# Kernel tuning notes

Hardware: AMD Instinct MI355X
Metric: run time of the kernel (lower is better)

## Reference

```python
import jax, jax.numpy as jnp
import numpy as np

D_MODEL = 1024
EXPAND = 2
D_INNER = D_MODEL * EXPAND  # 2048
C = 8
B, T = 4, 2048


def setup_inputs() -> dict:
    key = jax.random.key(0)
    ks = jax.random.split(key, 8)
    x = jax.random.normal(ks[0], (B, T, D_MODEL), jnp.float32)
    # omega init: uniform in [a, b] per the torch code
    a = np.log(1.0 / np.exp(np.log(0.999) / C) - 1.0)
    b = np.log(1.0 / np.exp(np.log(0.9) / C) - 1.0)
    omega = (a + (b - a) * jax.random.uniform(ks[1], (1, 1, D_INNER))).astype(jnp.float32)
    s = 0.02
    Win = (jax.random.normal(ks[2], (2 * D_INNER, D_MODEL)) * s).astype(jnp.float32)   # in_proj, no bias
    Wl = (jax.random.normal(ks[3], (D_INNER, D_INNER)) * s).astype(jnp.float32)        # lambda_proj weight
    bl = jnp.zeros((D_INNER,), jnp.float32)                                            # lambda_proj bias
    Wv = (jax.random.normal(ks[4], (D_INNER, D_INNER)) * s).astype(jnp.float32)        # mixer householder-vector proj
    bv = jnp.zeros((D_INNER,), jnp.float32)
    Wout = (jax.random.normal(ks[5], (D_MODEL, D_INNER)) * s).astype(jnp.float32)      # out_proj, no bias
    return dict(x=x, omega=omega, Win=Win, Wl=Wl, bl=bl, Wv=Wv, bv=bv, Wout=Wout)


def reference(x, omega, Win, Wl, bl, Wv, bv, Wout):
    # in_proj then split into (x, z)
    xz = jnp.einsum('btd,ed->bte', x, Win)              # [B,T,2*D_INNER]
    xi, z = jnp.split(xz, 2, axis=-1)                   # each [B,T,D_INNER]
    # lambda gate (computed for all timesteps at once)
    log_lam = -C * jax.nn.softplus(omega) * jax.nn.sigmoid(jnp.einsum('bti,ji->btj', xi, Wl) + bl)
    lam = jnp.exp(log_lam)                              # [B,T,D_INNER]
    # Householder (rank-1, identity activation) mixer vectors, hoisted out of the scan
    v = jnp.einsum('bti,ji->btj', xi, Wv) + bv          # [B,T,D_INNER]

    h0 = xi[:, 0]                                       # [B,D_INNER]

    def step(h_prev, inp):
        x_t, v_t, lam_t = inp
        vh = jnp.sum(v_t * h_prev, axis=-1, keepdims=True)
        vv = jnp.sum(v_t * v_t, axis=-1, keepdims=True)
        Qh = h_prev - 2.0 * v_t * (vh / vv)             # Householder reflection of h
        h = lam_t * Qh + (1.0 - lam_t) * x_t
        return h, h

    xs = (jnp.swapaxes(xi[:, 1:], 0, 1),                # [T-1,B,D_INNER]
          jnp.swapaxes(v[:, 1:], 0, 1),
          jnp.swapaxes(lam[:, 1:], 0, 1))
    _, hs = jax.lax.scan(step, h0, xs)                  # [T-1,B,D_INNER]
    h = jnp.concatenate([h0[:, None], jnp.swapaxes(hs, 0, 1)], axis=1)  # [B,T,D_INNER]

    return jnp.einsum('bti,di->btd', jax.nn.silu(z) * h, Wout)
```

## Files before the change

### kernel.cpp

```cpp
#include <hip/hip_runtime.h>
#include <cstdint>
#include <cstddef>

typedef unsigned short u16;
typedef __attribute__((ext_vector_type(8))) short s8v;
typedef __attribute__((ext_vector_type(4))) float f4v;
typedef __attribute__((ext_vector_type(2))) float f32x2;

#define D_MODEL 1024
#define D_INNER 2048
#define BT      8192
#define TLEN    2048
#define NBATCH  4

struct alignas(8) U16x4 { u16 x, y, z, w; };

__device__ __forceinline__ u16 f2bf(float f) {
  union { float f; unsigned u; } c; c.f = f;
  unsigned r = c.u + 0x7FFFu + ((c.u >> 16) & 1u);
  return (u16)(r >> 16);
}
__device__ __forceinline__ float blo(unsigned u) {
  union { unsigned u; float f; } c; c.u = u << 16; return c.f;
}
__device__ __forceinline__ float bhi(unsigned u) {
  union { unsigned u; float f; } c; c.u = u & 0xffff0000u; return c.f;
}
__device__ __forceinline__ unsigned pkbf(float lo, float hi) {
  union { float f; unsigned u; } a, b; a.f = lo; b.f = hi;
#if __has_builtin(__builtin_amdgcn_perm)
  return __builtin_amdgcn_perm(b.u + 0x8000u, a.u + 0x8000u, 0x07060302u);
#else
  return ((b.u + 0x8000u) & 0xffff0000u) | ((a.u + 0x8000u) >> 16);
#endif
}

#define DPPADD(x, ctrl) \
  ((x) + __builtin_bit_cast(float, __builtin_amdgcn_update_dpp( \
       0, __builtin_bit_cast(int, (x)), (ctrl), 0xF, 0xF, true)))
__device__ __forceinline__ float wave_sum_dpp(float x) {
  x = DPPADD(x, 0x111);
  x = DPPADD(x, 0x112);
  x = DPPADD(x, 0x114);
  x = DPPADD(x, 0x118);
  x = DPPADD(x, 0x142);
  x = DPPADD(x, 0x143);
  return x;
}

__device__ __forceinline__ void glds16(const u16* g, const u16* lds) {
  __builtin_amdgcn_global_load_lds(
      (const __attribute__((address_space(1))) unsigned int*)(uintptr_t)g,
      (__attribute__((address_space(3))) unsigned int*)(unsigned int)(uintptr_t)lds,
      16, 0, 0);
}

template<int EPI>
__global__ __launch_bounds__(256, 2)
void gemm_nt(const u16* __restrict__ A, const u16* __restrict__ B,
             int M, int N, int K,
             float* __restrict__ Cf, u16* __restrict__ Cb, u16* __restrict__ Cb2,
             const float* __restrict__ bias, const float* __restrict__ sfac,
             const float* __restrict__ bias2)
{
  __shared__ u16 lA[128 * 32];
  __shared__ u16 lB[128 * 32];
  const int tid  = threadIdx.x;
  const int wave = tid >> 6, lane = tid & 63;
  const int wm = wave >> 1, wn = wave & 1;
  const int bm0 = blockIdx.y * 128, bn0 = blockIdx.x * 128;

  const int srow = lane >> 2;
  const int scol = (lane & 3) * 8;
  const u16* pa0 = A + (size_t)(bm0 + wave * 32 + srow) * K + scol;
  const u16* pa1 = pa0 + (size_t)16 * K;
  const u16* pb0 = B + (size_t)(bn0 + wave * 32 + srow) * K + scol;
  const u16* pb1 = pb0 + (size_t)16 * K;
  u16* la0 = lA + (wave * 32) * 32;
  u16* la1 = la0 + 16 * 32;
  u16* lb0 = lB + (wave * 32) * 32;
  u16* lb1 = lb0 + 16 * 32;

  const int fr = lane & 15, kq = lane >> 4;
  const u16* fA = lA + (wm * 64 + fr) * 32 + kq * 8;
  const u16* fB = lB + (wn * 64 + fr) * 32 + kq * 8;

  f4v acc[4][4];
  const f4v zf = {0.f, 0.f, 0.f, 0.f};
  for (int i = 0; i < 4; ++i)
    for (int j = 0; j < 4; ++j)
      acc[i][j] = zf;

  for (int k0 = 0; k0 < K; k0 += 32) {
    glds16(pa0 + k0, la0);
    glds16(pa1 + k0, la1);
    glds16(pb0 + k0, lb0);
    glds16(pb1 + k0, lb1);
    __syncthreads();
    s8v af[4], bfv[4];
#pragma unroll
    for (int i = 0; i < 4; ++i) af[i] = *(const s8v*)(fA + i * 16 * 32);
#pragma unroll
    for (int j = 0; j < 4; ++j) bfv[j] = *(const s8v*)(fB + j * 16 * 32);
// ... 8 lines not shown
#pragma unroll
  for (int i = 0; i < 4; ++i) {
#pragma unroll
    for (int j = 0; j < 4; ++j) {
#pragma unroll
      for (int r = 0; r < 4; ++r) {
        const int gm = bm0 + wm * 64 + i * 16 + kq * 4 + r;
        const int gn = bn0 + wn * 64 + j * 16 + fr;
        const float val = acc[i][j][r];
        if (EPI == 0) {
          if (gn < D_INNER) {
            Cb[(size_t)gm * D_INNER + gn] = f2bf(val);
          } else {
            const float s = val / (1.f + __expf(-val));
            Cb2[(size_t)gm * D_INNER + (gn - D_INNER)] = f2bf(s);
          }
        } else if (EPI == 4) {
          if (gn < D_INNER) {
            const float pre = val + bias[gn];
            const float sig = 1.f / (1.f + __expf(-pre));
            const float m = -expm1f(sfac[gn] * sig);
            Cb2[(size_t)gm * D_INNER + gn] = f2bf(m);
          } else {
            Cb[(size_t)gm * D_INNER + (gn - D_INNER)] = f2bf(val + bias2[gn - D_INNER]);
          }
        } else {
          Cf[(size_t)gm * N + gn] = val;
        }
      }
    }
  }
}

__global__ void conv_bf16_kernel(const float* __restrict__ in, u16* __restrict__ out, int n4)
{
  const int i = blockIdx.x * blockDim.x + threadIdx.x;
  if (i >= n4) return;
  const float4 x = ((const float4*)in)[i];
  U16x4 o; o.x = f2bf(x.x); o.y = f2bf(x.y); o.z = f2bf(x.z); o.w = f2bf(x.w);
  ((U16x4*)out)[i] = o;
}

__global__ void sfac_kernel(const float* __restrict__ omega, float* __restrict__ sfac)
{
  const int i = blockIdx.x * blockDim.x + threadIdx.x;
  if (i < D_INNER) sfac[i] = -8.f * log1pf(expf(omega[i]));
}

__global__ __launch_bounds__(256)
void vscale_kernel(u16* __restrict__ v)
{
  const int row  = blockIdx.x * 4 + (threadIdx.x >> 6);
  const int lane = threadIdx.x & 63;
  uint4* p = (uint4*)(v + (size_t)row * D_INNER + lane * 32);
  uint4 a[4];
#pragma unroll
  for (int i = 0; i < 4; ++i) a[i] = p[i];
  float s = 0.f;
#pragma unroll
  for (int i = 0; i < 4; ++i) {
    const unsigned w[4] = {a[i].x, a[i].y, a[i].z, a[i].w};
#pragma unroll
    for (int j = 0; j < 4; ++j) {
      const float f0 = blo(w[j]), f1 = bhi(w[j]);
      s += f0 * f0 + f1 * f1;
    }
  }
  s += __shfl_down(s, 32); s += __shfl_down(s, 16); s += __shfl_down(s, 8);
  s += __shfl_down(s, 4);  s += __shfl_down(s, 2);  s += __shfl_down(s, 1);
  const float sc = sqrtf(2.f / __shfl(s, 0));
#pragma unroll
  for (int i = 0; i < 4; ++i) {
    const unsigned w[4] = {a[i].x, a[i].y, a[i].z, a[i].w};
    unsigned o[4];
#pragma unroll
    for (int j = 0; j < 4; ++j) o[j] = pkbf(blo(w[j]) * sc, bhi(w[j]) * sc);
    uint4 ov; ov.x = o[0]; ov.y = o[1]; ov.z = o[2]; ov.w = o[3];
    p[i] = ov;
  }
}

__global__ __launch_bounds__(256)
void pairprep_kernel(const u16* __restrict__ vs, const u16* __restrict__ mb,
                     const u16* __restrict__ xi, f32x2* __restrict__ C12)
{
  const int r = blockIdx.x * 4 + (threadIdx.x >> 6);
  const int lane = threadIdx.x & 63;
  const int b = r >> 10;
  const int t = (r & 1023) * 2;
  const size_t o0 = ((size_t)b * TLEN + t) * D_INNER + (size_t)lane * 32;
  const size_t o1 = o0 + D_INNER;
  const uint4* pv0 = (const uint4*)(vs + o0);
  const uint4* pv1 = (const uint4*)(vs + o1);
  const uint4* px0 = (const uint4*)(xi + o0);
  const uint4* pm0 = (const uint4*)(mb + o0);
  float c1 = 0.f, c2 = 0.f;
#pragma unroll
  for (int i = 0; i < 4; ++i) {
    const uint4 v0 = pv0[i], v1 = pv1[i], x0 = px0[i], m0 = pm0[i];
    const unsigned v0w[4] = {v0.x, v0.y, v0.z, v0.w};
    const unsigned v1w[4] = {v1.x, v1.y, v1.z, v1.w};
    const unsigned x0w[4] = {x0.x, x0.y, x0.z, x0.w};
    const unsigned m0w[4] = {m0.x, m0.y, m0.z, m0.w};
#pragma unroll
    for (int q = 0; q < 4; ++q) {
      const float va = blo(v0w[q]), vb = bhi(v0w[q]);
      const float ua = blo(v1w[q]), ub = bhi(v1w[q]);
      const float xa = blo(x0w[q]), xb = bhi(x0w[q]);
      const float ma = blo(m0w[q]), mbv = bhi(m0w[q]);
      const float wa = __builtin_fmaf(-ua, ma, ua);
      const float wb = __builtin_fmaf(-ub, mbv, ub);
      c1 += wa * va + wb * vb;
      c2 += ua * (ma * xa) + ub * (mbv * xb);
    }
  }
  c1 = wave_sum_dpp(c1);
  c2 = wave_sum_dpp(c2);
  if (lane == 63) { f32x2 cc; cc.x = c1; cc.y = c2; C12[r] = cc; }
}

__global__ void zmul_kernel(u16* __restrict__ gh, const u16* __restrict__ sz, int n8)
{
  const int i = blockIdx.x * blockDim.x + threadIdx.x;
  if (i >= n8) return;
  const uint4 hv = ((const uint4*)gh)[i];
  const uint4 zv = ((const uint4*)sz)[i];
  const unsigned hw[4] = {hv.x, hv.y, hv.z, hv.w};
  const unsigned zw[4] = {zv.x, zv.y, zv.z, zv.w};
  unsigned ow[4];
#pragma unroll
  for (int q = 0; q < 4; ++q)
    ow[q] = pkbf(blo(zw[q]) * blo(hw[q]), bhi(zw[q]) * bhi(hw[q]));
  uint4 o; o.x = ow[0]; o.y = ow[1]; o.z = ow[2]; o.w = ow[3];
  ((uint4*)gh)[i] = o;
}

struct Pair {
  uint4 v0, v1, x0, x1, m0, m1;
  f32x2 c;
};

__global__ __launch_bounds__(256, 1)
void scan2_kernel(const u16* __restrict__ xi, const u16* __restrict__ vs,
                  const u16* __restrict__ mb, const f32x2* __restrict__ C12,
                  u16* __restrict__ hb)
{
  const int b = blockIdx.x, tid = threadIdx.x;
  const int wave = tid >> 6, lane = tid & 63;
  const size_t base = (size_t)b * TLEN * D_INNER + (size_t)tid * 8;
  const int cb0 = b * 1024;
  __shared__ __attribute__((aligned(16))) float rP[2][4], rQ[2][4];

  auto load_pair = [&](int t) {
    Pair p;
    const size_t o0 = base + (size_t)t * D_INNER;
    const size_t o1 = o0 + D_INNER;
    p.v0 = *(const uint4*)(vs + o0);
    p.v1 = *(const uint4*)(vs + o1);
    p.x0 = *(const uint4*)(xi + o0);
    p.x1 = *(const uint4*)(xi + o1);
    p.m0 = *(const uint4*)(mb + o0);
    p.m1 = *(const uint4*)(mb + o1);
    p.c = C12[cb0 + (t >> 1)];
    return p;
  };

  float h[8];
  {
    const uint4 x0 = *(const uint4*)(xi + base);
    const unsigned xw[4] = {x0.x, x0.y, x0.z, x0.w};
#pragma unroll
    for (int p = 0; p < 4; ++p) {
      h[2*p]   = blo(xw[p]);
      h[2*p+1] = bhi(xw[p]);
    }
    *(uint4*)(hb + base) = x0;
  }

  {
    const size_t o = base + D_INNER;
    const uint4 v1v = *(const uint4*)(vs + o);
    const uint4 x1v = *(const uint4*)(xi + o);
    const uint4 m1v = *(const uint4*)(mb + o);
    const unsigned vw[4] = {v1v.x, v1v.y, v1v.z, v1v.w};
    float vf[8];
    float P0 = 0.f, P1 = 0.f;
#pragma unroll
    for (int p = 0; p < 4; ++p) {
      vf[2*p]   = blo(vw[p]);
      vf[2*p+1] = bhi(vw[p]);
      P0 = __builtin_fmaf(vf[2*p],   h[2*p],   P0);
      P1 = __builtin_fmaf(vf[2*p+1], h[2*p+1], P1);
    }
    float P = wave_sum_dpp(P0 + P1);
    if (lane == 63) rP[0][wave] = P;
    asm volatile("s_waitcnt lgkmcnt(0)\n\ts_barrier" ::: "memory");
    const float4 sp = *(const float4*)rP[0];
    const float a = (sp.x + sp.y) + (sp.z + sp.w);
    const unsigned xw[4] = {x1v.x, x1v.y, x1v.z, x1v.w};
    const unsigned mw[4] = {m1v.x, m1v.y, m1v.z, m1v.w};
    unsigned ow[4];
#pragma unroll
    for (int p = 0; p < 4; ++p) {
      const float X0 = blo(xw[p]), X1 = bhi(xw[p]);
      const float M0 = blo(mw[p]), M1 = bhi(mw[p]);
      const float t0 = __builtin_fmaf(vf[2*p],   -a, h[2*p]);
      const float t1 = __builtin_fmaf(vf[2*p+1], -a, h[2*p+1]);
      h[2*p]   = __builtin_fmaf(M0, X0 - t0, t0);
      h[2*p+1] = __builtin_fmaf(M1, X1 - t1, t1);
      ow[p] = pkbf(h[2*p], h[2*p+1]);
    }
    uint4 out; out.x = ow[0]; out.y = ow[1]; out.z = ow[2]; out.w = ow[3];
    *(uint4*)(hb + o) = out;
  }

  auto round = [&](const Pair& p, int t) {
    const int par = (t >> 1) & 1;
    const unsigned v0w[4] = {p.v0.x, p.v0.y, p.v0.z, p.v0.w};
    const unsigned v1w[4] = {p.v1.x, p.v1.y, p.v1.z, p.v1.w};
    const unsigned m0w[4] = {p.m0.x, p.m0.y, p.m0.z, p.m0.w};
    float vf[8], uf[8], mf0[8];
    float P0 = 0.f, P1 = 0.f, Q0 = 0.f, Q1 = 0.f;
#pragma unroll
    for (int q = 0; q < 4; ++q) {
      vf[2*q]   = blo(v0w[q]);
      vf[2*q+1] = bhi(v0w[q]);
      uf[2*q]   = blo(v1w[q]);
      uf[2*q+1] = bhi(v1w[q]);
      mf0[2*q]  = blo(m0w[q]);
      mf0[2*q+1]= bhi(m0w[q]);
      const float wa = __builtin_fmaf(-uf[2*q],   mf0[2*q],   uf[2*q]);
      const float wb = __builtin_fmaf(-uf[2*q+1], mf0[2*q+1], uf[2*q+1]);
      P0 = __builtin_fmaf(vf[2*q],   h[2*q],   P0);
      P1 = __builtin_fmaf(vf[2*q+1], h[2*q+1], P1);
      Q0 = __builtin_fmaf(wa, h[2*q],   Q0);
      Q1 = __builtin_fmaf(wb, h[2*q+1], Q1);
    }
    float P = wave_sum_dpp(P0 + P1);
    float Q = wave_sum_dpp(Q0 + Q1);
    if (lane == 63) { rP[par][wave] = P; rQ[par][wave] = Q; }
    asm volatile("s_waitcnt lgkmcnt(0)\n\ts_barrier" ::: "memory");
    const float4 sp = *(const float4*)rP[par];
    const float4 sq = *(const float4*)rQ[par];
    const float a0 = (sp.x + sp.y) + (sp.z + sp.w);
    const float a1 = __builtin_fmaf(-a0, p.c.x, (sq.x + sq.y) + (sq.z + sq.w) + p.c.y);
    const unsigned xw0[4] = {p.x0.x, p.x0.y, p.x0.z, p.x0.w};
    const unsigned xw1[4] = {p.x1.x, p.x1.y, p.x1.z, p.x1.w};
    const unsigned m1w[4] = {p.m1.x, p.m1.y, p.m1.z, p.m1.w};
    unsigned ow0[4], ow1[4];
#pragma unroll
    for (int q = 0; q < 4; ++q) {
      const float A0 = blo(xw0[q]), A1 = bhi(xw0[q]);
      const float B0 = blo(xw1[q]), B1 = bhi(xw1[q]);
      const float N0 = blo(m1w[q]), N1 = bhi(m1w[q]);
      float t0 = __builtin_fmaf(vf[2*q],   -a0, h[2*q]);
      float t1 = __builtin_fmaf(vf[2*q+1], -a0, h[2*q+1]);
      t0 = __builtin_fmaf(mf0[2*q],   A0 - t0, t0);
      t1 = __builtin_fmaf(mf0[2*q+1], A1 - t1, t1);
      ow0[q] = pkbf(t0, t1);
      const float u0 = __builtin_fmaf(uf[2*q],   -a1, t0);
      const float u1 = __builtin_fmaf(uf[2*q+1], -a1, t1);
      h[2*q]   = __builtin_fmaf(N0, B0 - u0, u0);
      h[2*q+1] = __builtin_fmaf(N1, B1 - u1, u1);
      ow1[q] = pkbf(h[2*q], h[2*q+1]);
    }
    const size_t oo = base + (size_t)t * D_INNER;
    uint4 o0; o0.x = ow0[0]; o0.y = ow0[1]; o0.z = ow0[2]; o0.w = ow0[3];
    uint4 o1; o1.x = ow1[0]; o1.y = ow1[1]; o1.z = ow1[2]; o1.w = ow1[3];
    *(uint4*)(hb + oo) = o0;
    *(uint4*)(hb + oo + D_INNER) = o1;
  };

  Pair A = load_pair(2);
  __builtin_amdgcn_sched_barrier(0);
  Pair B = load_pair(4);
  __builtin_amdgcn_sched_barrier(0);
  for (int t = 2; t <= 2038; t += 4) {
    Pair An = load_pair(t + 4);
    __builtin_amdgcn_sched_barrier(0);
    round(A, t);
    A = An;
    Pair Bn = load_pair(t + 6);
    __builtin_amdgcn_sched_barrier(0);
    round(B, t + 2);
    B = Bn;
  }
  {
    Pair An = load_pair(2046);
    __builtin_amdgcn_sched_barrier(0);
    round(A, 2042);
    round(B, 2044);
    round(An, 2046);
  }
}

extern "C" void kernel_launch(void* const* d_in, const int* in_sizes, int n_in,
                              void* d_out, int out_size, void* d_ws, size_t ws_size,
                              hipStream_t stream)
{
  const float* x     = (const float*)d_in[0];
  const float* omega = (const float*)d_in[1];
  const float* Win   = (const float*)d_in[2];
  const float* Wl    = (const float*)d_in[3];
  const float* bl    = (const float*)d_in[4];
  const float* Wv    = (const float*)d_in[5];
  const float* bv    = (const float*)d_in[6];
  const float* Wout  = (const float*)d_in[7];
  float* out = (float*)d_out;
  (void)in_sizes; (void)n_in; (void)out_size; (void)ws_size;

  size_t off = 0;
  auto carve = [&](size_t bytes) -> void* {
    void* r = (char*)d_ws + off;
    off += (bytes + 255) & ~(size_t)255;
    return r;
  };
  u16*  x_bf    = (u16*)carve((size_t)BT * D_MODEL * 2);
  u16*  Win_bf  = (u16*)carve((size_t)2 * D_INNER * D_MODEL * 2);
  u16*  Wl_bf   = (u16*)carve((size_t)D_INNER * D_INNER * 2);
  u16*  Wv_bf   = (u16*)carve((size_t)D_INNER * D_INNER * 2);
  u16*  Wout_bf = (u16*)carve((size_t)D_MODEL * D_INNER * 2);
  u16*  xi_bf   = (u16*)carve((size_t)BT * D_INNER * 2);
  u16*  sz_bf   = (u16*)carve((size_t)BT * D_INNER * 2);
  u16*  v_bf    = (u16*)carve((size_t)BT * D_INNER * 2);
  u16*  gh_bf   = (u16*)carve((size_t)BT * D_INNER * 2);
  u16*  mb      = (u16*)carve((size_t)BT * D_INNER * 2);
  float* sfac   = (float*)carve((size_t)D_INNER * 4);
  f32x2* C12    = (f32x2*)carve((size_t)(BT / 2) * 8);

  conv_bf16_kernel<<<(BT * D_MODEL / 4 + 255) / 256, 256, 0, stream>>>(x, x_bf, BT * D_MODEL / 4);
  conv_bf16_kernel<<<(2 * D_INNER * D_MODEL / 4 + 255) / 256, 256, 0, stream>>>(Win, Win_bf, 2 * D_INNER * D_MODEL / 4);
  conv_bf16_kernel<<<(D_INNER * D_INNER / 4 + 255) / 256, 256, 0, stream>>>(Wl, Wl_bf, D_INNER * D_INNER / 4);
  conv_bf16_kernel<<<(D_INNER * D_INNER / 4 + 255) / 256, 256, 0, stream>>>(Wv, Wv_bf, D_INNER * D_INNER / 4);
  conv_bf16_kernel<<<(D_MODEL * D_INNER / 4 + 255) / 256, 256, 0, stream>>>(Wout, Wout_bf, D_MODEL * D_INNER / 4);
  sfac_kernel<<<(D_INNER + 255) / 256, 256, 0, stream>>>(omega, sfac);

  gemm_nt<0><<<dim3(4096 / 128, BT / 128), 256, 0, stream>>>(
      x_bf, Win_bf, BT, 4096, D_MODEL, nullptr, xi_bf, sz_bf, nullptr, nullptr, nullptr);
  gemm_nt<4><<<dim3(4096 / 128, BT / 128), 256, 0, stream>>>(
      xi_bf, Wl_bf, BT, 4096, D_INNER, nullptr, v_bf, mb, bl, sfac, bv);
  vscale_kernel<<<BT / 4, 256, 0, stream>>>(v_bf);
  pairprep_kernel<<<BT / 2 / 4, 256, 0, stream>>>(v_bf, mb, xi_bf, C12);
  scan2_kernel<<<NBATCH, 256, 0, stream>>>(xi_bf, v_bf, mb, C12, gh_bf);
  zmul_kernel<<<(BT * D_INNER / 8 + 255) / 256, 256, 0, stream>>>(gh_bf, sz_bf, BT * D_INNER / 8);
  gemm_nt<3><<<dim3(D_MODEL / 128, BT / 128), 256, 0, stream>>>(
      gh_bf, Wout_bf, BT, D_MODEL, D_INNER, out, nullptr, nullptr, nullptr, nullptr, nullptr);
}
```

Baseline: 1.088 ms.

## Block the sequential Householder scan into 8-step chunks with precomputed coupling coefficients

The sequential scan previously advanced two timesteps per block-wide barrier, using per-pair coefficients from a prep kernel. It now advances eight timesteps per barrier. A new prep kernel precomputes a lower-triangular set of 28 coupling coefficients plus 7 offset terms per 8-step block, and the scan solves an 8x8 triangular system after a single reduction. This cuts the number of barriers and dependent reductions in the latency-bound scan by about four times. In exchange it adds a heavier, register-hungry prep kernel, larger per-iteration register state in the scan (possible spills at one wave per SIMD), and different fp rounding.

```diff
diff --git a/kernel.cpp b/kernel.cpp
--- a/kernel.cpp
+++ b/kernel.cpp
@@ -5,13 +5,14 @@
 typedef unsigned short u16;
 typedef __attribute__((ext_vector_type(8))) short s8v;
 typedef __attribute__((ext_vector_type(4))) float f4v;
-typedef __attribute__((ext_vector_type(2))) float f32x2;
 
 #define D_MODEL 1024
 #define D_INNER 2048
 #define BT      8192
 #define TLEN    2048
 #define NBATCH  4
+#define BSLOT   256
+#define NBLK    255
 
 struct alignas(8) U16x4 { u16 x, y, z, w; };
 
@@ -192,42 +193,95 @@
 }
 
 __global__ __launch_bounds__(256)
-void pairprep_kernel(const u16* __restrict__ vs, const u16* __restrict__ mb,
-                     const u16* __restrict__ xi, f32x2* __restrict__ C12)
+void blockprep_kernel(const u16* __restrict__ vs, const u16* __restrict__ mb,
+                      const u16* __restrict__ xi, float4* __restrict__ cf)
 {
   const int r = blockIdx.x * 4 + (threadIdx.x >> 6);
   const int lane = threadIdx.x & 63;
-  const int b = r >> 10;
-  const int t = (r & 1023) * 2;
-  const size_t o0 = ((size_t)b * TLEN + t) * D_INNER + (size_t)lane * 32;
-  const size_t o1 = o0 + D_INNER;
-  const uint4* pv0 = (const uint4*)(vs + o0);
-  const uint4* pv1 = (const uint4*)(vs + o1);
-  const uint4* px0 = (const uint4*)(xi + o0);
-  const uint4* pm0 = (const uint4*)(mb + o0);
-  float c1 = 0.f, c2 = 0.f;
+  const int b = r >> 8;
+  const int q = r & (BSLOT - 1);
+  if (q >= NBLK) return;
+  const size_t e = ((size_t)b * TLEN + 8 * q + 1) * D_INNER + (size_t)lane * 32;
+
+  float cacc[8][8];
+  float dacc[8];
+#pragma unroll
+  for (int j = 0; j < 8; ++j) {
+    dacc[j] = 0.f;
+#pragma unroll
+    for (int k = 0; k < 8; ++k) cacc[j][k] = 0.f;
+  }
+
 #pragma unroll
   for (int i = 0; i < 4; ++i) {
-    const uint4 v0 = pv0[i], v1 = pv1[i], x0 = px0[i], m0 = pm0[i];
-    const unsigned v0w[4] = {v0.x, v0.y, v0.z, v0.w};
-    const unsigned v1w[4] = {v1.x, v1.y, v1.z, v1.w};
-    const unsigned x0w[4] = {x0.x, x0.y, x0.z, x0.w};
-    const unsigned m0w[4] = {m0.x, m0.y, m0.z, m0.w};
-#pragma unroll
-    for (int q = 0; q < 4; ++q) {
-      const float va = blo(v0w[q]), vb = bhi(v0w[q]);
-      const float ua = blo(v1w[q]), ub = bhi(v1w[q]);
-      const float xa = blo(x0w[q]), xb = bhi(x0w[q]);
-      const float ma = blo(m0w[q]), mbv = bhi(m0w[q]);
-      const float wa = __builtin_fmaf(-ua, ma, ua);
-      const float wb = __builtin_fmaf(-ub, mbv, ub);
-      c1 += wa * va + wb * vb;
-      c2 += ua * (ma * xa) + ub * (mbv * xb);
-    }
-  }
-  c1 = wave_sum_dpp(c1);
-  c2 = wave_sum_dpp(c2);
-  if (lane == 63) { f32x2 cc; cc.x = c1; cc.y = c2; C12[r] = cc; }
+    float a[7][8];
+    float B[8], pl[8], py[8];
+#pragma unroll
+    for (int ch = 0; ch < 8; ++ch) B[ch] = 0.f;
+#pragma unroll
+    for (int jj = 0; jj < 8; ++jj) {
+      const size_t o = e + (size_t)jj * D_INNER + i * 8;
+      const uint4 vq = *(const uint4*)(vs + o);
+      const uint4 mq = *(const uint4*)(mb + o);
+      const uint4 xq = *(const uint4*)(xi + o);
+      const unsigned vw[4] = {vq.x, vq.y, vq.z, vq.w};
+      const unsigned mw[4] = {mq.x, mq.y, mq.z, mq.w};
+      const unsigned xw[4] = {xq.x, xq.y, xq.z, xq.w};
+      float vf[8], mf[8], xf[8], lf[8];
+#pragma unroll
+      for (int k = 0; k < 4; ++k) {
+        vf[2*k] = blo(vw[k]); vf[2*k+1] = bhi(vw[k]);
+        mf[2*k] = blo(mw[k]); mf[2*k+1] = bhi(mw[k]);
+        xf[2*k] = blo(xw[k]); xf[2*k+1] = bhi(xw[k]);
+        lf[2*k] = 1.f - mf[2*k]; lf[2*k+1] = 1.f - mf[2*k+1];
+      }
+      if (jj > 0) {
+        float dd = 0.f;
+#pragma unroll
+        for (int ch = 0; ch < 8; ++ch) {
+          B[ch] = __builtin_fmaf(pl[ch], B[ch], py[ch]);
+          dd = __builtin_fmaf(vf[ch], B[ch], dd);
+        }
+        dacc[jj] += dd;
+#pragma unroll
+        for (int k = 0; k < jj; ++k) {
+          float cc = 0.f;
+#pragma unroll
+          for (int ch = 0; ch < 8; ++ch)
+            cc = __builtin_fmaf(vf[ch], a[k][ch], cc);
+          cacc[jj][k] += cc;
+#pragma unroll
+          for (int ch = 0; ch < 8; ++ch) a[k][ch] *= lf[ch];
+        }
+      }
+      if (jj < 7) {
+#pragma unroll
+        for (int ch = 0; ch < 8; ++ch) a[jj][ch] = lf[ch] * vf[ch];
+      }
+#pragma unroll
+      for (int ch = 0; ch < 8; ++ch) { pl[ch] = lf[ch]; py[ch] = mf[ch] * xf[ch]; }
+    }
+  }
+
+#pragma unroll
+  for (int jj = 1; jj < 8; ++jj) {
+    dacc[jj] = wave_sum_dpp(dacc[jj]);
+#pragma unroll
+    for (int k = 0; k < jj; ++k) cacc[jj][k] = wave_sum_dpp(cacc[jj][k]);
+  }
+  if (lane == 63) {
+    float4* o = cf + (size_t)r * 9;
+    float4 f;
+    f.x = cacc[1][0]; f.y = cacc[2][0]; f.z = cacc[2][1]; f.w = cacc[3][0]; o[0] = f;
+    f.x = cacc[3][1]; f.y = cacc[3][2]; f.z = cacc[4][0]; f.w = cacc[4][1]; o[1] = f;
+    f.x = cacc[4][2]; f.y = cacc[4][3]; f.z = cacc[5][0]; f.w = cacc[5][1]; o[2] = f;
+    f.x = cacc[5][2]; f.y = cacc[5][3]; f.z = cacc[5][4]; f.w = cacc[6][0]; o[3] = f;
+    f.x = cacc[6][1]; f.y = cacc[6][2]; f.z = cacc[6][3]; f.w = cacc[6][4]; o[4] = f;
+    f.x = cacc[6][5]; f.y = cacc[7][0]; f.z = cacc[7][1]; f.w = cacc[7][2]; o[5] = f;
+    f.x = cacc[7][3]; f.y = cacc[7][4]; f.z = cacc[7][5]; f.w = cacc[7][6]; o[6] = f;
+    f.x = dacc[1];    f.y = dacc[2];    f.z = dacc[3];    f.w = dacc[4];    o[7] = f;
+    f.x = dacc[5];    f.y = dacc[6];    f.z = dacc[7];    f.w = 0.f;        o[8] = f;
+  }
 }
 
 __global__ void zmul_kernel(u16* __restrict__ gh, const u16* __restrict__ sz, int n8)
@@ -246,33 +300,33 @@
   ((uint4*)gh)[i] = o;
 }
 
-struct Pair {
-  uint4 v0, v1, x0, x1, m0, m1;
-  f32x2 c;
+struct Blk {
+  uint4 v[8], x[8], m[8];
+  float4 c[9];
 };
 
 __global__ __launch_bounds__(256, 1)
-void scan2_kernel(const u16* __restrict__ xi, const u16* __restrict__ vs,
-                  const u16* __restrict__ mb, const f32x2* __restrict__ C12,
+void scan8_kernel(const u16* __restrict__ xi, const u16* __restrict__ vs,
+                  const u16* __restrict__ mb, const float4* __restrict__ cf,
                   u16* __restrict__ hb)
 {
   const int b = blockIdx.x, tid = threadIdx.x;
   const int wave = tid >> 6, lane = tid & 63;
   const size_t base = (size_t)b * TLEN * D_INNER + (size_t)tid * 8;
-  const int cb0 = b * 1024;
-  __shared__ __attribute__((aligned(16))) float rP[2][4], rQ[2][4];
-
-  auto load_pair = [&](int t) {
-    Pair p;
-    const size_t o0 = base + (size_t)t * D_INNER;
-    const size_t o1 = o0 + D_INNER;
-    p.v0 = *(const uint4*)(vs + o0);
-    p.v1 = *(const uint4*)(vs + o1);
-    p.x0 = *(const uint4*)(xi + o0);
-    p.x1 = *(const uint4*)(xi + o1);
-    p.m0 = *(const uint4*)(mb + o0);
-    p.m1 = *(const uint4*)(mb + o1);
-    p.c = C12[cb0 + (t >> 1)];
+  __shared__ __attribute__((aligned(16))) float sS[2][8][4];
+
+  auto load_blk = [&](int q) {
+    Blk p;
+    const size_t e1 = base + (size_t)(8 * q + 1) * D_INNER;
+#pragma unroll
+    for (int j = 0; j < 8; ++j) {
+      p.v[j] = *(const uint4*)(vs + e1 + (size_t)j * D_INNER);
+      p.x[j] = *(const uint4*)(xi + e1 + (size_t)j * D_INNER);
+      p.m[j] = *(const uint4*)(mb + e1 + (size_t)j * D_INNER);
+    }
+    const float4* cp = cf + (size_t)(b * BSLOT + q) * 9;
+#pragma unroll
+    for (int i = 0; i < 9; ++i) p.c[i] = cp[i];
     return p;
   };
 
@@ -288,121 +342,135 @@
     *(uint4*)(hb + base) = x0;
   }
 
-  {
-    const size_t o = base + D_INNER;
-    const uint4 v1v = *(const uint4*)(vs + o);
-    const uint4 x1v = *(const uint4*)(xi + o);
-    const uint4 m1v = *(const uint4*)(mb + o);
-    const unsigned vw[4] = {v1v.x, v1v.y, v1v.z, v1v.w};
-    float vf[8];
+  auto round = [&](const Blk& p, int q) {
+    const int par = q & 1;
+    float h0g[8];
+#pragma unroll
+    for (int k = 0; k < 8; ++k) h0g[k] = h[k];
+    float P[8];
+#pragma unroll
+    for (int j = 0; j < 8; ++j) {
+      const unsigned vw[4] = {p.v[j].x, p.v[j].y, p.v[j].z, p.v[j].w};
+      float a0 = 0.f, a1 = 0.f;
+#pragma unroll
+      for (int k = 0; k < 4; ++k) {
+        a0 = __builtin_fmaf(blo(vw[k]), h0g[2*k],   a0);
+        a1 = __builtin_fmaf(bhi(vw[k]), h0g[2*k+1], a1);
+      }
+      P[j] = a0 + a1;
+      if (j < 7) {
+        const unsigned mw[4] = {p.m[j].x, p.m[j].y, p.m[j].z, p.m[j].w};
+#pragma unroll
+        for (int k = 0; k < 4; ++k) {
+          h0g[2*k]   *= (1.f - blo(mw[k]));
+          h0g[2*k+1] *= (1.f - bhi(mw[k]));
+        }
+      }
+    }
+#pragma unroll
+    for (int j = 0; j < 8; ++j) {
+      P[j] = wave_sum_dpp(P[j]);
+      if (lane == 63) sS[par][j][wave] = P[j];
+    }
+    asm volatile("s_waitcnt lgkmcnt(0)\n\ts_barrier" ::: "memory");
+    float S[8];
+#pragma unroll
+    for (int j = 0; j < 8; ++j) {
+      const float4 sp = *(const float4*)&sS[par][j][0];
+      S[j] = (sp.x + sp.y) + (sp.z + sp.w);
+    }
+    const float c21 = p.c[0].x, c31 = p.c[0].y, c32 = p.c[0].z, c41 = p.c[0].w;
+    const float c42 = p.c[1].x, c43 = p.c[1].y, c51 = p.c[1].z, c52 = p.c[1].w;
+    const float c53 = p.c[2].x, c54 = p.c[2].y, c61 = p.c[2].z, c62 = p.c[2].w;
+    const float c63 = p.c[3].x, c64 = p.c[3].y, c65 = p.c[3].z, c71 = p.c[3].w;
+    const float c72 = p.c[4].x, c73 = p.c[4].y, c74 = p.c[4].z, c75 = p.c[4].w;
+    const float c76 = p.c[5].x, c81 = p.c[5].y, c82 = p.c[5].z, c83 = p.c[5].w;
+    const float c84 = p.c[6].x, c85 = p.c[6].y, c86 = p.c[6].z, c87 = p.c[6].w;
+    const float d2 = p.c[7].x, d3 = p.c[7].y, d4 = p.c[7].z, d5 = p.c[7].w;
+    const float d6 = p.c[8].x, d7 = p.c[8].y, d8 = p.c[8].z;
+    float sv[8];
+    sv[0] = S[0];
+    sv[1] = __builtin_fmaf(-c21, sv[0], S[1] + d2);
+    sv[2] = __builtin_fmaf(-c32, sv[1], __builtin_fmaf(-c31, sv[0], S[2] + d3));
+    sv[3] = __builtin_fmaf(-c43, sv[2], __builtin_fmaf(-c42, sv[1],
+              __builtin_fmaf(-c41, sv[0], S[3] + d4)));
+    sv[4] = __builtin_fmaf(-c54, sv[3], __builtin_fmaf(-c53, sv[2],
+              __builtin_fmaf(-c52, sv[1], __builtin_fmaf(-c51, sv[0], S[4] + d5))));
+    sv[5] = __builtin_fmaf(-c65, sv[4], __builtin_fmaf(-c64, sv[3],
+              __builtin_fmaf(-c63, sv[2], __builtin_fmaf(-c62, sv[1],
+              __builtin_fmaf(-c61, sv[0], S[5] + d6)))));
+    sv[6] = __builtin_fmaf(-c76, sv[5], __builtin_fmaf(-c75, sv[4],
+              __builtin_fmaf(-c74, sv[3], __builtin_fmaf(-c73, sv[2],
+              __builtin_fmaf(-c72, sv[1], __builtin_fmaf(-c71, sv[0], S[6] + d7))))));
+    sv[7] = __builtin_fmaf(-c87, sv[6], __builtin_fmaf(-c86, sv[5],
+              __builtin_fmaf(-c85, sv[4], __builtin_fmaf(-c84, sv[3],
+              __builtin_fmaf(-c83, sv[2], __builtin_fmaf(-c82, sv[1],
+              __builtin_fmaf(-c81, sv[0], S[7] + d8)))))));
+    const size_t e1 = base + (size_t)(8 * q + 1) * D_INNER;
+#pragma unroll
+    for (int j = 0; j < 8; ++j) {
+      const unsigned vw[4] = {p.v[j].x, p.v[j].y, p.v[j].z, p.v[j].w};
+      const unsigned mw[4] = {p.m[j].x, p.m[j].y, p.m[j].z, p.m[j].w};
+      const unsigned xw[4] = {p.x[j].x, p.x[j].y, p.x[j].z, p.x[j].w};
+      unsigned ow[4];
+#pragma unroll
+      for (int k = 0; k < 4; ++k) {
+        const float X0 = blo(xw[k]), X1 = bhi(xw[k]);
+        const float t0 = __builtin_fmaf(blo(vw[k]), -sv[j], h[2*k]);
+        const float t1 = __builtin_fmaf(bhi(vw[k]), -sv[j], h[2*k+1]);
+        h[2*k]   = __builtin_fmaf(blo(mw[k]), X0 - t0, t0);
+        h[2*k+1] = __builtin_fmaf(bhi(mw[k]), X1 - t1, t1);
+        ow[k] = pkbf(h[2*k], h[2*k+1]);
+      }
+      uint4 o; o.x = ow[0]; o.y = ow[1]; o.z = ow[2]; o.w = ow[3];
+      *(uint4*)(hb + e1 + (size_t)j * D_INNER) = o;
+    }
+  };
+
+  auto solo = [&](int t, int par) {
+    const size_t o = base + (size_t)t * D_INNER;
+    const uint4 vv = *(const uint4*)(vs + o);
+    const uint4 xv = *(const uint4*)(xi + o);
+    const uint4 mv = *(const uint4*)(mb + o);
+    const unsigned vw[4] = {vv.x, vv.y, vv.z, vv.w};
     float P0 = 0.f, P1 = 0.f;
 #pragma unroll
-    for (int p = 0; p < 4; ++p) {
-      vf[2*p]   = blo(vw[p]);
-      vf[2*p+1] = bhi(vw[p]);
-      P0 = __builtin_fmaf(vf[2*p],   h[2*p],   P0);
-      P1 = __builtin_fmaf(vf[2*p+1], h[2*p+1], P1);
+    for (int k = 0; k < 4; ++k) {
+      P0 = __builtin_fmaf(blo(vw[k]), h[2*k],   P0);
+      P1 = __builtin_fmaf(bhi(vw[k]), h[2*k+1], P1);
     }
     float P = wave_sum_dpp(P0 + P1);
-    if (lane == 63) rP[0][wave] = P;
+    if (lane == 63) sS[par][0][wave] = P;
     asm volatile("s_waitcnt lgkmcnt(0)\n\ts_barrier" ::: "memory");
-    const float4 sp = *(const float4*)rP[0];
-    const float a = (sp.x + sp.y) + (sp.z + sp.w);
-    const unsigned xw[4] = {x1v.x, x1v.y, x1v.z, x1v.w};
-    const unsigned mw[4] = {m1v.x, m1v.y, m1v.z, m1v.w};
+    const float4 sp = *(const float4*)&sS[par][0][0];
+    const float s = (sp.x + sp.y) + (sp.z + sp.w);
+    const unsigned xw[4] = {xv.x, xv.y, xv.z, xv.w};
+    const unsigned mw[4] = {mv.x, mv.y, mv.z, mv.w};
     unsigned ow[4];
 #pragma unroll
-    for (int p = 0; p < 4; ++p) {
-      const float X0 = blo(xw[p]), X1 = bhi(xw[p]);
-      const float M0 = blo(mw[p]), M1 = bhi(mw[p]);
-      const float t0 = __builtin_fmaf(vf[2*p],   -a, h[2*p]);
-      const float t1 = __builtin_fmaf(vf[2*p+1], -a, h[2*p+1]);
-      h[2*p]   = __builtin_fmaf(M0, X0 - t0, t0);
-      h[2*p+1] = __builtin_fmaf(M1, X1 - t1, t1);
-      ow[p] = pkbf(h[2*p], h[2*p+1]);
-    }
-    uint4 out; out.x = ow[0]; out.y = ow[1]; out.z = ow[2]; out.w = ow[3];
-    *(uint4*)(hb + o) = out;
-  }
-
-  auto round = [&](const Pair& p, int t) {
-    const int par = (t >> 1) & 1;
-    const unsigned v0w[4] = {p.v0.x, p.v0.y, p.v0.z, p.v0.w};
-    const unsigned v1w[4] = {p.v1.x, p.v1.y, p.v1.z, p.v1.w};
-    const unsigned m0w[4] = {p.m0.x, p.m0.y, p.m0.z, p.m0.w};
-    float vf[8], uf[8], mf0[8];
-    float P0 = 0.f, P1 = 0.f, Q0 = 0.f, Q1 = 0.f;
-#pragma unroll
-    for (int q = 0; q < 4; ++q) {
-      vf[2*q]   = blo(v0w[q]);
-      vf[2*q+1] = bhi(v0w[q]);
-      uf[2*q]   = blo(v1w[q]);
-      uf[2*q+1] = bhi(v1w[q]);
-      mf0[2*q]  = blo(m0w[q]);
-      mf0[2*q+1]= bhi(m0w[q]);
-      const float wa = __builtin_fmaf(-uf[2*q],   mf0[2*q],   uf[2*q]);
-      const float wb = __builtin_fmaf(-uf[2*q+1], mf0[2*q+1], uf[2*q+1]);
-      P0 = __builtin_fmaf(vf[2*q],   h[2*q],   P0);
-      P1 = __builtin_fmaf(vf[2*q+1], h[2*q+1], P1);
-      Q0 = __builtin_fmaf(wa, h[2*q],   Q0);
-      Q1 = __builtin_fmaf(wb, h[2*q+1], Q1);
-    }
-    float P = wave_sum_dpp(P0 + P1);
-    float Q = wave_sum_dpp(Q0 + Q1);
-    if (lane == 63) { rP[par][wave] = P; rQ[par][wave] = Q; }
-    asm volatile("s_waitcnt lgkmcnt(0)\n\ts_barrier" ::: "memory");
-    const float4 sp = *(const float4*)rP[par];
-    const float4 sq = *(const float4*)rQ[par];
-    const float a0 = (sp.x + sp.y) + (sp.z + sp.w);
-    const float a1 = __builtin_fmaf(-a0, p.c.x, (sq.x + sq.y) + (sq.z + sq.w) + p.c.y);
-    const unsigned xw0[4] = {p.x0.x, p.x0.y, p.x0.z, p.x0.w};
-    const unsigned xw1[4] = {p.x1.x, p.x1.y, p.x1.z, p.x1.w};
-    const unsigned m1w[4] = {p.m1.x, p.m1.y, p.m1.z, p.m1.w};
-    unsigned ow0[4], ow1[4];
-#pragma unroll
-    for (int q = 0; q < 4; ++q) {
-      const float A0 = blo(xw0[q]), A1 = bhi(xw0[q]);
-      const float B0 = blo(xw1[q]), B1 = bhi(xw1[q]);
-      const float N0 = blo(m1w[q]), N1 = bhi(m1w[q]);
-      float t0 = __builtin_fmaf(vf[2*q],   -a0, h[2*q]);
-      float t1 = __builtin_fmaf(vf[2*q+1], -a0, h[2*q+1]);
-      t0 = __builtin_fmaf(mf0[2*q],   A0 - t0, t0);
-      t1 = __builtin_fmaf(mf0[2*q+1], A1 - t1, t1);
-      ow0[q] = pkbf(t0, t1);
-      const float u0 = __builtin_fmaf(uf[2*q],   -a1, t0);
-      const float u1 = __builtin_fmaf(uf[2*q+1], -a1, t1);
-      h[2*q]   = __builtin_fmaf(N0, B0 - u0, u0);
-      h[2*q+1] = __builtin_fmaf(N1, B1 - u1, u1);
-      ow1[q] = pkbf(h[2*q], h[2*q+1]);
-    }
-    const size_t oo = base + (size_t)t * D_INNER;
-    uint4 o0; o0.x = ow0[0]; o0.y = ow0[1]; o0.z = ow0[2]; o0.w = ow0[3];
-    uint4 o1; o1.x = ow1[0]; o1.y = ow1[1]; o1.z = ow1[2]; o1.w = ow1[3];
-    *(uint4*)(hb + oo) = o0;
-    *(uint4*)(hb + oo + D_INNER) = o1;
+    for (int k = 0; k < 4; ++k) {
+      const float X0 = blo(xw[k]), X1 = bhi(xw[k]);
+      const float t0 = __builtin_fmaf(blo(vw[k]), -s, h[2*k]);
+      const float t1 = __builtin_fmaf(bhi(vw[k]), -s, h[2*k+1]);
+      h[2*k]   = __builtin_fmaf(blo(mw[k]), X0 - t0, t0);
+      h[2*k+1] = __builtin_fmaf(bhi(mw[k]), X1 - t1, t1);
+      ow[k] = pkbf(h[2*k], h[2*k+1]);
+    }
+    uint4 ov; ov.x = ow[0]; ov.y = ow[1]; ov.z = ow[2]; ov.w = ow[3];
+    *(uint4*)(hb + o) = ov;
   };
 
-  Pair A = load_pair(2);
+  Blk A = load_blk(0);
   __builtin_amdgcn_sched_barrier(0);
-  Pair B = load_pair(4);
-  __builtin_amdgcn_sched_barrier(0);
-  for (int t = 2; t <= 2038; t += 4) {
-    Pair An = load_pair(t + 4);
+  for (int q = 0; q < NBLK - 1; ++q) {
+    Blk N = load_blk(q + 1);
     __builtin_amdgcn_sched_barrier(0);
-    round(A, t);
-    A = An;
-    Pair Bn = load_pair(t + 6);
-    __builtin_amdgcn_sched_barrier(0);
-    round(B, t + 2);
-    B = Bn;
-  }
-  {
-    Pair An = load_pair(2046);
-    __builtin_amdgcn_sched_barrier(0);
-    round(A, 2042);
-    round(B, 2044);
-    round(An, 2046);
-  }
+    round(A, q);
+    A = N;
+  }
+  round(A, NBLK - 1);
+  solo(2041, 1); solo(2042, 0); solo(2043, 1); solo(2044, 0);
+  solo(2045, 1); solo(2046, 0); solo(2047, 1);
 }
 
 extern "C" void kernel_launch(void* const* d_in, const int* in_sizes, int n_in,
@@ -437,7 +505,7 @@
   u16*  gh_bf   = (u16*)carve((size_t)BT * D_INNER * 2);
   u16*  mb      = (u16*)carve((size_t)BT * D_INNER * 2);
   float* sfac   = (float*)carve((size_t)D_INNER * 4);
-  f32x2* C12    = (f32x2*)carve((size_t)(BT / 2) * 8);
+  float4* cf    = (float4*)carve((size_t)NBATCH * BSLOT * 9 * 16);
 
   conv_bf16_kernel<<<(BT * D_MODEL / 4 + 255) / 256, 256, 0, stream>>>(x, x_bf, BT * D_MODEL / 4);
   conv_bf16_kernel<<<(2 * D_INNER * D_MODEL / 4 + 255) / 256, 256, 0, stream>>>(Win, Win_bf, 2 * D_INNER * D_MODEL / 4);
@@ -451,8 +519,8 @@
   gemm_nt<4><<<dim3(4096 / 128, BT / 128), 256, 0, stream>>>(
       xi_bf, Wl_bf, BT, 4096, D_INNER, nullptr, v_bf, mb, bl, sfac, bv);
   vscale_kernel<<<BT / 4, 256, 0, stream>>>(v_bf);
-  pairprep_kernel<<<BT / 2 / 4, 256, 0, stream>>>(v_bf, mb, xi_bf, C12);
-  scan2_kernel<<<NBATCH, 256, 0, stream>>>(xi_bf, v_bf, mb, C12, gh_bf);
+  blockprep_kernel<<<NBATCH * BSLOT / 4, 256, 0, stream>>>(v_bf, mb, xi_bf, cf);
+  scan8_kernel<<<NBATCH, 256, 0, stream>>>(xi_bf, v_bf, mb, cf, gh_bf);
   zmul_kernel<<<(BT * D_INNER / 8 + 255) / 256, 256, 0, stream>>>(gh_bf, sz_bf, BT * D_INNER / 8);
   gemm_nt<3><<<dim3(D_MODEL / 128, BT / 128), 256, 0, stream>>>(
       gh_bf, Wout_bf, BT, D_MODEL, D_INNER, out, nullptr, nullptr, nullptr, nullptr, nullptr);
```

After: 1.252 ms. 1.15x slower.

## Widen scan to 512 threads, fuse bf16 conversions, use nontemporal scan stores

Applied to the files above, without the earlier changes.

The serial scan kernel now runs 512 threads per batch, so each thread holds 4 channels instead of 8 and the cross-wave reduction covers 8 waves. Its output stores become nontemporal. The five separate fp32-to-bf16 conversion launches are merged into one kernel that writes into the contiguous workspace. The aim is to shorten the latency-bound per-step critical path of the scan, which only uses 4 blocks, and to cut launch overhead, at the cost of a larger barrier and reduction per step.

```diff
diff --git a/kernel.cpp b/kernel.cpp
--- a/kernel.cpp
+++ b/kernel.cpp
@@ -6,6 +6,7 @@
 typedef __attribute__((ext_vector_type(8))) short s8v;
 typedef __attribute__((ext_vector_type(4))) float f4v;
 typedef __attribute__((ext_vector_type(2))) float f32x2;
+typedef __attribute__((ext_vector_type(2))) unsigned u32x2;
 
 #define D_MODEL 1024
 #define D_INNER 2048
@@ -143,13 +144,27 @@
   }
 }
 
-__global__ void conv_bf16_kernel(const float* __restrict__ in, u16* __restrict__ out, int n4)
-{
-  const int i = blockIdx.x * blockDim.x + threadIdx.x;
-  if (i >= n4) return;
-  const float4 x = ((const float4*)in)[i];
-  U16x4 o; o.x = f2bf(x.x); o.y = f2bf(x.y); o.z = f2bf(x.z); o.w = f2bf(x.w);
-  ((U16x4*)out)[i] = o;
+#define CV_R0 2097152
+#define CV_R1 3145728
+#define CV_R2 4194304
+#define CV_R3 5242880
+#define CV_R4 5767168
+
+__global__ __launch_bounds__(256)
+void convall_kernel(const float* __restrict__ x, const float* __restrict__ Win,
+                    const float* __restrict__ Wl, const float* __restrict__ Wv,
+                    const float* __restrict__ Wout, u16* __restrict__ outb)
+{
+  const int g = blockIdx.x * 256 + threadIdx.x;
+  const float* in; int lo;
+  if (g < CV_R0)      { in = x;    lo = g; }
+  else if (g < CV_R1) { in = Win;  lo = g - CV_R0; }
+  else if (g < CV_R2) { in = Wl;   lo = g - CV_R1; }
+  else if (g < CV_R3) { in = Wv;   lo = g - CV_R2; }
+  else                { in = Wout; lo = g - CV_R3; }
+  const float4 v = ((const float4*)in)[lo];
+  U16x4 o; o.x = f2bf(v.x); o.y = f2bf(v.y); o.z = f2bf(v.z); o.w = f2bf(v.w);
+  ((U16x4*)outb)[g] = o;
 }
 
 __global__ void sfac_kernel(const float* __restrict__ omega, float* __restrict__ sfac)
@@ -247,93 +262,90 @@
 }
 
 struct Pair {
-  uint4 v0, v1, x0, x1, m0, m1;
+  uint2 v0, v1, x0, x1, m0, m1;
   f32x2 c;
 };
 
-__global__ __launch_bounds__(256, 1)
+__global__ __launch_bounds__(512, 1)
 void scan2_kernel(const u16* __restrict__ xi, const u16* __restrict__ vs,
                   const u16* __restrict__ mb, const f32x2* __restrict__ C12,
                   u16* __restrict__ hb)
 {
   const int b = blockIdx.x, tid = threadIdx.x;
   const int wave = tid >> 6, lane = tid & 63;
-  const size_t base = (size_t)b * TLEN * D_INNER + (size_t)tid * 8;
+  const size_t base = (size_t)b * TLEN * D_INNER + (size_t)tid * 4;
   const int cb0 = b * 1024;
-  __shared__ __attribute__((aligned(16))) float rP[2][4], rQ[2][4];
+  __shared__ __attribute__((aligned(16))) float rP[2][8], rQ[2][8];
 
   auto load_pair = [&](int t) {
     Pair p;
     const size_t o0 = base + (size_t)t * D_INNER;
     const size_t o1 = o0 + D_INNER;
-    p.v0 = *(const uint4*)(vs + o0);
-    p.v1 = *(const uint4*)(vs + o1);
-    p.x0 = *(const uint4*)(xi + o0);
-    p.x1 = *(const uint4*)(xi + o1);
-    p.m0 = *(const uint4*)(mb + o0);
-    p.m1 = *(const uint4*)(mb + o1);
+    p.v0 = *(const uint2*)(vs + o0);
+    p.v1 = *(const uint2*)(vs + o1);
+    p.x0 = *(const uint2*)(xi + o0);
+    p.x1 = *(const uint2*)(xi + o1);
+    p.m0 = *(const uint2*)(mb + o0);
+    p.m1 = *(const uint2*)(mb + o1);
     p.c = C12[cb0 + (t >> 1)];
     return p;
   };
 
-  float h[8];
+  float h[4];
   {
-    const uint4 x0 = *(const uint4*)(xi + base);
-    const unsigned xw[4] = {x0.x, x0.y, x0.z, x0.w};
-#pragma unroll
-    for (int p = 0; p < 4; ++p) {
-      h[2*p]   = blo(xw[p]);
-      h[2*p+1] = bhi(xw[p]);
-    }
-    *(uint4*)(hb + base) = x0;
+    const uint2 x0 = *(const uint2*)(xi + base);
+    h[0] = blo(x0.x); h[1] = bhi(x0.x); h[2] = blo(x0.y); h[3] = bhi(x0.y);
+    u32x2 o; o.x = x0.x; o.y = x0.y;
+    __builtin_nontemporal_store(o, (u32x2*)(hb + base));
   }
 
   {
     const size_t o = base + D_INNER;
-    const uint4 v1v = *(const uint4*)(vs + o);
-    const uint4 x1v = *(const uint4*)(xi + o);
-    const uint4 m1v = *(const uint4*)(mb + o);
-    const unsigned vw[4] = {v1v.x, v1v.y, v1v.z, v1v.w};
-    float vf[8];
+    const uint2 v1v = *(const uint2*)(vs + o);
+    const uint2 x1v = *(const uint2*)(xi + o);
+    const uint2 m1v = *(const uint2*)(mb + o);
+    const unsigned vw[2] = {v1v.x, v1v.y};
+    float vf[4];
     float P0 = 0.f, P1 = 0.f;
 #pragma unroll
-    for (int p = 0; p < 4; ++p) {
-      vf[2*p]   = blo(vw[p]);
-      vf[2*p+1] = bhi(vw[p]);
-      P0 = __builtin_fmaf(vf[2*p],   h[2*p],   P0);
-      P1 = __builtin_fmaf(vf[2*p+1], h[2*p+1], P1);
+    for (int q = 0; q < 2; ++q) {
+      vf[2*q]   = blo(vw[q]);
+      vf[2*q+1] = bhi(vw[q]);
+      P0 = __builtin_fmaf(vf[2*q],   h[2*q],   P0);
+      P1 = __builtin_fmaf(vf[2*q+1], h[2*q+1], P1);
     }
     float P = wave_sum_dpp(P0 + P1);
     if (lane == 63) rP[0][wave] = P;
     asm volatile("s_waitcnt lgkmcnt(0)\n\ts_barrier" ::: "memory");
-    const float4 sp = *(const float4*)rP[0];
-    const float a = (sp.x + sp.y) + (sp.z + sp.w);
-    const unsigned xw[4] = {x1v.x, x1v.y, x1v.z, x1v.w};
-    const unsigned mw[4] = {m1v.x, m1v.y, m1v.z, m1v.w};
-    unsigned ow[4];
-#pragma unroll
-    for (int p = 0; p < 4; ++p) {
-      const float X0 = blo(xw[p]), X1 = bhi(xw[p]);
-      const float M0 = blo(mw[p]), M1 = bhi(mw[p]);
-      const float t0 = __builtin_fmaf(vf[2*p],   -a, h[2*p]);
-      const float t1 = __builtin_fmaf(vf[2*p+1], -a, h[2*p+1]);
-      h[2*p]   = __builtin_fmaf(M0, X0 - t0, t0);
-      h[2*p+1] = __builtin_fmaf(M1, X1 - t1, t1);
-      ow[p] = pkbf(h[2*p], h[2*p+1]);
-    }
-    uint4 out; out.x = ow[0]; out.y = ow[1]; out.z = ow[2]; out.w = ow[3];
-    *(uint4*)(hb + o) = out;
+    const float4 pa = *(const float4*)&rP[0][0];
+    const float4 pb = *(const float4*)&rP[0][4];
+    const float a = ((pa.x + pa.y) + (pa.z + pa.w)) + ((pb.x + pb.y) + (pb.z + pb.w));
+    const unsigned xw[2] = {x1v.x, x1v.y};
+    const unsigned mw[2] = {m1v.x, m1v.y};
+    unsigned ow[2];
+#pragma unroll
+    for (int q = 0; q < 2; ++q) {
+      const float X0 = blo(xw[q]), X1 = bhi(xw[q]);
+      const float M0 = blo(mw[q]), M1 = bhi(mw[q]);
+      const float t0 = __builtin_fmaf(vf[2*q],   -a, h[2*q]);
+      const float t1 = __builtin_fmaf(vf[2*q+1], -a, h[2*q+1]);
+      h[2*q]   = __builtin_fmaf(M0, X0 - t0, t0);
+      h[2*q+1] = __builtin_fmaf(M1, X1 - t1, t1);
+      ow[q] = pkbf(h[2*q], h[2*q+1]);
+    }
+    u32x2 ov; ov.x = ow[0]; ov.y = ow[1];
+    __builtin_nontemporal_store(ov, (u32x2*)(hb + o));
   }
 
   auto round = [&](const Pair& p, int t) {
     const int par = (t >> 1) & 1;
-    const unsigned v0w[4] = {p.v0.x, p.v0.y, p.v0.z, p.v0.w};
-    const unsigned v1w[4] = {p.v1.x, p.v1.y, p.v1.z, p.v1.w};
-    const unsigned m0w[4] = {p.m0.x, p.m0.y, p.m0.z, p.m0.w};
-    float vf[8], uf[8], mf0[8];
+    const unsigned v0w[2] = {p.v0.x, p.v0.y};
+    const unsigned v1w[2] = {p.v1.x, p.v1.y};
+    const unsigned m0w[2] = {p.m0.x, p.m0.y};
+    float vf[4], uf[4], mf0[4];
     float P0 = 0.f, P1 = 0.f, Q0 = 0.f, Q1 = 0.f;
 #pragma unroll
-    for (int q = 0; q < 4; ++q) {
+    for (int q = 0; q < 2; ++q) {
       vf[2*q]   = blo(v0w[q]);
       vf[2*q+1] = bhi(v0w[q]);
       uf[2*q]   = blo(v1w[q]);
@@ -351,16 +363,19 @@
     float Q = wave_sum_dpp(Q0 + Q1);
     if (lane == 63) { rP[par][wave] = P; rQ[par][wave] = Q; }
     asm volatile("s_waitcnt lgkmcnt(0)\n\ts_barrier" ::: "memory");
-    const float4 sp = *(const float4*)rP[par];
-    const float4 sq = *(const float4*)rQ[par];
-    const float a0 = (sp.x + sp.y) + (sp.z + sp.w);
-    const float a1 = __builtin_fmaf(-a0, p.c.x, (sq.x + sq.y) + (sq.z + sq.w) + p.c.y);
-    const unsigned xw0[4] = {p.x0.x, p.x0.y, p.x0.z, p.x0.w};
-    const unsigned xw1[4] = {p.x1.x, p.x1.y, p.x1.z, p.x1.w};
-    const unsigned m1w[4] = {p.m1.x, p.m1.y, p.m1.z, p.m1.w};
-    unsigned ow0[4], ow1[4];
-#pragma unroll
-    for (int q = 0; q < 4; ++q) {
+    const float4 pa = *(const float4*)&rP[par][0];
+    const float4 pb = *(const float4*)&rP[par][4];
+    const float4 qa = *(const float4*)&rQ[par][0];
+    const float4 qb = *(const float4*)&rQ[par][4];
+    const float a0 = ((pa.x + pa.y) + (pa.z + pa.w)) + ((pb.x + pb.y) + (pb.z + pb.w));
+    const float sQ = ((qa.x + qa.y) + (qa.z + qa.w)) + ((qb.x + qb.y) + (qb.z + qb.w));
+    const float a1 = __builtin_fmaf(-a0, p.c.x, sQ + p.c.y);
+    const unsigned xw0[2] = {p.x0.x, p.x0.y};
+    const unsigned xw1[2] = {p.x1.x, p.x1.y};
+    const unsigned m1w[2] = {p.m1.x, p.m1.y};
+    unsigned ow0[2], ow1[2];
+#pragma unroll
+    for (int q = 0; q < 2; ++q) {
       const float A0 = blo(xw0[q]), A1 = bhi(xw0[q]);
       const float B0 = blo(xw1[q]), B1 = bhi(xw1[q]);
       const float N0 = blo(m1w[q]), N1 = bhi(m1w[q]);
@@ -376,10 +391,10 @@
       ow1[q] = pkbf(h[2*q], h[2*q+1]);
     }
     const size_t oo = base + (size_t)t * D_INNER;
-    uint4 o0; o0.x = ow0[0]; o0.y = ow0[1]; o0.z = ow0[2]; o0.w = ow0[3];
-    uint4 o1; o1.x = ow1[0]; o1.y = ow1[1]; o1.z = ow1[2]; o1.w = ow1[3];
-    *(uint4*)(hb + oo) = o0;
-    *(uint4*)(hb + oo + D_INNER) = o1;
+    u32x2 o0; o0.x = ow0[0]; o0.y = ow0[1];
+    u32x2 o1; o1.x = ow1[0]; o1.y = ow1[1];
+    __builtin_nontemporal_store(o0, (u32x2*)(hb + oo));
+    __builtin_nontemporal_store(o1, (u32x2*)(hb + oo + D_INNER));
   };
 
   Pair A = load_pair(2);
@@ -439,11 +454,7 @@
   float* sfac   = (float*)carve((size_t)D_INNER * 4);
   f32x2* C12    = (f32x2*)carve((size_t)(BT / 2) * 8);
 
-  conv_bf16_kernel<<<(BT * D_MODEL / 4 + 255) / 256, 256, 0, stream>>>(x, x_bf, BT * D_MODEL / 4);
-  conv_bf16_kernel<<<(2 * D_INNER * D_MODEL / 4 + 255) / 256, 256, 0, stream>>>(Win, Win_bf, 2 * D_INNER * D_MODEL / 4);
-  conv_bf16_kernel<<<(D_INNER * D_INNER / 4 + 255) / 256, 256, 0, stream>>>(Wl, Wl_bf, D_INNER * D_INNER / 4);
-  conv_bf16_kernel<<<(D_INNER * D_INNER / 4 + 255) / 256, 256, 0, stream>>>(Wv, Wv_bf, D_INNER * D_INNER / 4);
-  conv_bf16_kernel<<<(D_MODEL * D_INNER / 4 + 255) / 256, 256, 0, stream>>>(Wout, Wout_bf, D_MODEL * D_INNER / 4);
+  convall_kernel<<<CV_R4 / 256, 256, 0, stream>>>(x, Win, Wl, Wv, Wout, x_bf);
   sfac_kernel<<<(D_INNER + 255) / 256, 256, 0, stream>>>(omega, sfac);
 
   gemm_nt<0><<<dim3(4096 / 128, BT / 128), 256, 0, stream>>>(
@@ -452,7 +463,7 @@
       xi_bf, Wl_bf, BT, 4096, D_INNER, nullptr, v_bf, mb, bl, sfac, bv);
   vscale_kernel<<<BT / 4, 256, 0, stream>>>(v_bf);
   pairprep_kernel<<<BT / 2 / 4, 256, 0, stream>>>(v_bf, mb, xi_bf, C12);
-  scan2_kernel<<<NBATCH, 256, 0, stream>>>(xi_bf, v_bf, mb, C12, gh_bf);
+  scan2_kernel<<<NBATCH, 512, 0, stream>>>(xi_bf, v_bf, mb, C12, gh_bf);
   zmul_kernel<<<(BT * D_INNER / 8 + 255) / 256, 256, 0, stream>>>(gh_bf, sz_bf, BT * D_INNER / 8);
   gemm_nt<3><<<dim3(D_MODEL / 128, BT / 128), 256, 0, stream>>>(
       gh_bf, Wout_bf, BT, D_MODEL, D_INNER, out, nullptr, nullptr, nullptr, nullptr, nullptr);
```

Result: slower. 1.164 ms (+7.0%).

## Remap GEMM workgroups across XCDs and merge bf16 conversions into one kernel

Applied to the files above, without the earlier changes.

The GEMM now remaps its linear workgroup id so that consecutive tiles land on the same XCD (stride-8 interleave). The goal is more L2 reuse of A and B tiles across chiplets. The five separate fp32-to-bf16 conversion launches are also merged into a single kernel that relies on the converted buffers being laid out back to back in the workspace. This saves launch overhead but depends on the 256-byte carve alignment keeping those buffers contiguous.

```diff
diff --git a/kernel.cpp b/kernel.cpp
--- a/kernel.cpp
+++ b/kernel.cpp
@@ -68,7 +68,12 @@
   const int tid  = threadIdx.x;
   const int wave = tid >> 6, lane = tid & 63;
   const int wm = wave >> 1, wn = wave & 1;
-  const int bm0 = blockIdx.y * 128, bn0 = blockIdx.x * 128;
+
+  const int nwg = (int)(gridDim.x * gridDim.y);
+  int wg = (int)(blockIdx.y * gridDim.x + blockIdx.x);
+  wg = (wg & 7) * (nwg >> 3) + (wg >> 3);
+  const int bm0 = (wg / (int)gridDim.x) * 128;
+  const int bn0 = (wg % (int)gridDim.x) * 128;
 
   const int srow = lane >> 2;
   const int scol = (lane & 3) * 8;
@@ -143,13 +148,27 @@
   }
 }
 
-__global__ void conv_bf16_kernel(const float* __restrict__ in, u16* __restrict__ out, int n4)
-{
-  const int i = blockIdx.x * blockDim.x + threadIdx.x;
-  if (i >= n4) return;
-  const float4 x = ((const float4*)in)[i];
-  U16x4 o; o.x = f2bf(x.x); o.y = f2bf(x.y); o.z = f2bf(x.z); o.w = f2bf(x.w);
-  ((U16x4*)out)[i] = o;
+#define CV_R0 2097152
+#define CV_R1 3145728
+#define CV_R2 4194304
+#define CV_R3 5242880
+#define CV_R4 5767168
+
+__global__ __launch_bounds__(256)
+void convall_kernel(const float* __restrict__ x, const float* __restrict__ Win,
+                    const float* __restrict__ Wl, const float* __restrict__ Wv,
+                    const float* __restrict__ Wout, u16* __restrict__ outb)
+{
+  const int g = blockIdx.x * 256 + threadIdx.x;
+  const float* in; int lo;
+  if (g < CV_R0)      { in = x;    lo = g; }
+  else if (g < CV_R1) { in = Win;  lo = g - CV_R0; }
+  else if (g < CV_R2) { in = Wl;   lo = g - CV_R1; }
+  else if (g < CV_R3) { in = Wv;   lo = g - CV_R2; }
+  else                { in = Wout; lo = g - CV_R3; }
+  const float4 v = ((const float4*)in)[lo];
+  U16x4 o; o.x = f2bf(v.x); o.y = f2bf(v.y); o.z = f2bf(v.z); o.w = f2bf(v.w);
+  ((U16x4*)outb)[g] = o;
 }
 
 __global__ void sfac_kernel(const float* __restrict__ omega, float* __restrict__ sfac)
@@ -439,11 +458,7 @@
   float* sfac   = (float*)carve((size_t)D_INNER * 4);
   f32x2* C12    = (f32x2*)carve((size_t)(BT / 2) * 8);
 
-  conv_bf16_kernel<<<(BT * D_MODEL / 4 + 255) / 256, 256, 0, stream>>>(x, x_bf, BT * D_MODEL / 4);
-  conv_bf16_kernel<<<(2 * D_INNER * D_MODEL / 4 + 255) / 256, 256, 0, stream>>>(Win, Win_bf, 2 * D_INNER * D_MODEL / 4);
-  conv_bf16_kernel<<<(D_INNER * D_INNER / 4 + 255) / 256, 256, 0, stream>>>(Wl, Wl_bf, D_INNER * D_INNER / 4);
-  conv_bf16_kernel<<<(D_INNER * D_INNER / 4 + 255) / 256, 256, 0, stream>>>(Wv, Wv_bf, D_INNER * D_INNER / 4);
-  conv_bf16_kernel<<<(D_MODEL * D_INNER / 4 + 255) / 256, 256, 0, stream>>>(Wout, Wout_bf, D_MODEL * D_INNER / 4);
+  convall_kernel<<<CV_R4 / 256, 256, 0, stream>>>(x, Win, Wl, Wv, Wout, x_bf);
   sfac_kernel<<<(D_INNER + 255) / 256, 256, 0, stream>>>(omega, sfac);
 
   gemm_nt<0><<<dim3(4096 / 128, BT / 128), 256, 0, stream>>>(
```

After: 1.070 ms. No clear change (-1.6%).
